# Kernel optimization log

Hardware: AMD Instinct MI355X
Metric: run time of the kernel (lower is better)

Reference implementation:

```python
import jax, jax.numpy as jnp
import numpy as np

D_IN = 1024
D_OUT = 1024

def setup_inputs() -> dict:
    key = jax.random.key(0)
    kx, kq, kk, kv = jax.random.split(key, 4)
    scale = 1.0 / np.sqrt(D_IN)
    return {
        "x": jax.random.normal(kx, (4, 4096, D_IN), dtype=jnp.float32),
        "W_q": jax.random.uniform(kq, (D_IN, D_OUT), dtype=jnp.float32, minval=-scale, maxval=scale),
        "W_k": jax.random.uniform(kk, (D_IN, D_OUT), dtype=jnp.float32, minval=-scale, maxval=scale),
        "W_v": jax.random.uniform(kv, (D_IN, D_OUT), dtype=jnp.float32, minval=-scale, maxval=scale),
    }

def reference(x, W_q, W_k, W_v):
    # x: [b, s, d_in]; weights stored as [d_in, d_out] (transposed vs torch Linear)
    Q = jnp.einsum('bsd,de->bse', x, W_q)
    K = jnp.einsum('bsd,de->bse', x, W_k)
    V = jnp.einsum('bsd,de->bse', x, W_v)
    d_k = K.shape[-1]
    scores = jnp.einsum('bqe,bke->bqk', Q, K) / jnp.sqrt(jnp.asarray(d_k, x.dtype))
    weights = jax.nn.softmax(scores, axis=-1)
    return jnp.einsum('bqk,bke->bqe', weights, V)
```

## Files before the change

kernel.cpp:

```cpp
#include <hip/hip_runtime.h>

typedef unsigned short u16;
typedef float f32x4 __attribute__((ext_vector_type(4)));
typedef u16   u16x4 __attribute__((ext_vector_type(4)));
typedef u16   u16x8 __attribute__((ext_vector_type(8)));
typedef __bf16 bf16x8 __attribute__((ext_vector_type(8)));

static __device__ __forceinline__ u16 f2bf(float x) {
    unsigned int u = __builtin_bit_cast(unsigned int, x);
    u = (u + 0x7FFFu + ((u >> 16) & 1u)) >> 16;
    return (u16)u;
}
static __device__ __forceinline__ bf16x8 as_bf(u16x8 v) { return __builtin_bit_cast(bf16x8, v); }

static __device__ __forceinline__ void gload16(const u16* g, u16* lds) {
    __builtin_amdgcn_global_load_lds(
        (const __attribute__((address_space(1))) void*)g,
        (__attribute__((address_space(3))) void*)lds,
        16, 0, 0);
}

#define KSCALE 0.045084220027780106f

#define STAGE_G2L(dst, src, stride, ROUNDS) do {                               \
    _Pragma("unroll") for (int i_ = 0; i_ < (ROUNDS); ++i_) {                  \
        int c_ = (i_ * 4 + w) * 64 + l;                                        \
        int row_ = c_ >> 3, c8_ = c_ & 7;                                      \
        gload16((src) + (size_t)row_ * (stride) + ((c8_ ^ (row_ & 7)) << 3),   \
                &(dst)[(i_ * 4 + w) * 512]);                                   \
    } } while (0)

__global__ __launch_bounds__(256) void wt_kernel(const float* __restrict__ Wq,
                                                 const float* __restrict__ Wk,
                                                 const float* __restrict__ Wv,
                                                 u16* __restrict__ Wt) {
    __shared__ float tile[64][65];
    const int mat = blockIdx.z;
    const float* W = (mat == 0) ? Wq : ((mat == 1) ? Wk : Wv);
    const int bx = blockIdx.x, by = blockIdx.y;
    const int tid = threadIdx.x;
#pragma unroll
    for (int i = 0; i < 16; ++i) {
        int idx = i * 256 + tid;
        int r = idx >> 6, c = idx & 63;
        tile[r][c] = W[(by * 64 + r) * 1024 + bx * 64 + c];
    }
    __syncthreads();
#pragma unroll
    for (int i = 0; i < 16; ++i) {
        int idx = i * 256 + tid;
        int r = idx >> 6, c = idx & 63;
        Wt[mat * 1048576 + (bx * 64 + r) * 1024 + by * 64 + c] = f2bf(tile[c][r]);
    }
}

__global__ __launch_bounds__(256, 3) void qkv_gemm(const float* __restrict__ X,
                                                   const u16* __restrict__ Wt,
                                                   u16* __restrict__ Qo,
                                                   u16* __restrict__ Ko,
                                                   u16* __restrict__ Vt) {
    __shared__ u16 As[128 * 64];
    __shared__ u16 Bs[128 * 64];
    const int bid = blockIdx.x;
    const int swz = (bid & 7) * 96 + (bid >> 3);
    const int bm = swz / 24, bn = swz % 24;
    const int tid = threadIdx.x;
    const int w = tid >> 6, l = tid & 63, lg = l >> 4, lr = l & 15;
    const int wr = w >> 1, wc = w & 1;

    const f32x4 z4 = {0.f, 0.f, 0.f, 0.f};
    f32x4 acc[4][4];
#pragma unroll
    for (int m = 0; m < 4; ++m)
#pragma unroll
        for (int n = 0; n < 4; ++n) acc[m][n] = z4;

    for (int kb = 0; kb < 16; ++kb) {
        __syncthreads();
        STAGE_G2L(Bs, Wt + (size_t)(bn * 128) * 1024 + kb * 64, 1024, 4);
#pragma unroll
        for (int i = 0; i < 4; ++i) {
            int cid = i * 256 + tid;
            int row = cid >> 3, c8 = cid & 7;
            const float* src = X + (bm * 128 + row) * 1024 + kb * 64 + c8 * 8;
            f32x4 v0 = *(const f32x4*)(src);
            f32x4 v1 = *(const f32x4*)(src + 4);
            u16x8 t;
            t[0] = f2bf(v0[0]); t[1] = f2bf(v0[1]); t[2] = f2bf(v0[2]); t[3] = f2bf(v0[3]);
            t[4] = f2bf(v1[0]); t[5] = f2bf(v1[1]); t[6] = f2bf(v1[2]); t[7] = f2bf(v1[3]);
            *(u16x8*)(&As[row * 64 + ((c8 ^ (row & 7)) << 3)]) = t;
        }
        __syncthreads();
#pragma unroll
        for (int kk = 0; kk < 2; ++kk) {
            bf16x8 af[4], bfr[4];
#pragma unroll
            for (int m = 0; m < 4; ++m) {
                int row = wr * 64 + m * 16 + lr;
                af[m] = as_bf(*(const u16x8*)(&As[row * 64 + (((kk * 4 + lg) ^ (lr & 7)) << 3)]));
            }
#pragma unroll
            for (int n = 0; n < 4; ++n) {
                int row = wc * 64 + n * 16 + lr;
                bfr[n] = as_bf(*(const u16x8*)(&Bs[row * 64 + (((kk * 4 + lg) ^ (lr & 7)) << 3)]));
            }
#pragma unroll
            for (int m = 0; m < 4; ++m)
#pragma unroll
                for (int n = 0; n < 4; ++n)
                    acc[m][n] = __builtin_amdgcn_mfma_f32_16x16x32_bf16(af[m], bfr[n], acc[m][n], 0, 0, 0);
        }
    }
    const int row0 = bm * 128 + wr * 64;
    const int col0 = bn * 128 + wc * 64;
#pragma unroll
    for (int m = 0; m < 4; ++m) {
#pragma unroll
        for (int n = 0; n < 4; ++n) {
            int col = col0 + n * 16 + lr;
            int mat = col >> 10;
            int cg = col & 1023;
            int row = row0 + m * 16 + lg * 4;
            if (mat == 2) {
                u16x4 v;
                v[0] = f2bf(acc[m][n][0]); v[1] = f2bf(acc[m][n][1]);
                v[2] = f2bf(acc[m][n][2]); v[3] = f2bf(acc[m][n][3]);
                *(u16x4*)(Vt + cg * 4096 + row) = v;
            } else {
                u16* P = mat ? Ko : Qo;
#pragma unroll
                for (int r = 0; r < 4; ++r) P[(row + r) * 1024 + cg] = f2bf(acc[m][n][r]);
            }
        }
    }
}

__global__ __launch_bounds__(256, 4) void qk_gemm(const u16* __restrict__ Qb,
                                                  const u16* __restrict__ Kb,
                                                  u16* __restrict__ P) {
    __shared__ u16 As[128 * 64];
    __shared__ u16 Bs[128 * 64];
    const int bid = blockIdx.x;
    const int swz = (bid & 7) * 128 + (bid >> 3);
    const int bm = swz >> 5, bn = swz & 31;
    const int tid = threadIdx.x;
    const int w = tid >> 6, l = tid & 63, lg = l >> 4, lr = l & 15;
    const int wr = w >> 1, wc = w & 1;

    const f32x4 z4 = {0.f, 0.f, 0.f, 0.f};
    f32x4 acc[4][4];
#pragma unroll
    for (int m = 0; m < 4; ++m)
#pragma unroll
        for (int n = 0; n < 4; ++n) acc[m][n] = z4;

    for (int kb = 0; kb < 16; ++kb) {
        __syncthreads();
        STAGE_G2L(As, Qb + (size_t)(bm * 128) * 1024 + kb * 64, 1024, 4);
        STAGE_G2L(Bs, Kb + (size_t)(bn * 128) * 1024 + kb * 64, 1024, 4);
        __syncthreads();
#pragma unroll
        for (int kk = 0; kk < 2; ++kk) {
            bf16x8 af[4], bfr[4];
#pragma unroll
            for (int m = 0; m < 4; ++m) {
                int row = wr * 64 + m * 16 + lr;
                af[m] = as_bf(*(const u16x8*)(&As[row * 64 + (((kk * 4 + lg) ^ (lr & 7)) << 3)]));
            }
#pragma unroll
            for (int n = 0; n < 4; ++n) {
                int row = wc * 64 + n * 16 + lr;
                bfr[n] = as_bf(*(const u16x8*)(&Bs[row * 64 + (((kk * 4 + lg) ^ (lr & 7)) << 3)]));
            }
#pragma unroll
            for (int m = 0; m < 4; ++m)
#pragma unroll
                for (int n = 0; n < 4; ++n)
                    acc[m][n] = __builtin_amdgcn_mfma_f32_16x16x32_bf16(af[m], bfr[n], acc[m][n], 0, 0, 0);
        }
    }
    const int row0 = bm * 128 + wr * 64;
    const int col0 = bn * 128 + wc * 64;
#pragma unroll
    for (int m = 0; m < 4; ++m) {
#pragma unroll
        for (int r = 0; r < 4; ++r) {
            const size_t rowg = (size_t)(row0 + m * 16 + lg * 4 + r);
#pragma unroll
            for (int n = 0; n < 4; ++n)
                P[rowg * 4096 + col0 + n * 16 + lr] = f2bf(exp2f(acc[m][n][r] * KSCALE));
        }
    }
}

__global__ __launch_bounds__(256, 4) void pv_pair(const u16* __restrict__ P0,
                                                  const u16* __restrict__ P1,
                                                  const u16* __restrict__ V0,
                                                  const u16* __restrict__ V1,
                                                  float* __restrict__ Out0,
                                                  float* __restrict__ Out1) {
    __shared__ u16 As[128 * 64];
    __shared__ u16 Bs[128 * 64];
    const int bid = blockIdx.x;
    const int swz = (bid & 7) * 64 + (bid >> 3);
    const int bb = swz >> 8, rem = swz & 255;
    const int bm = rem >> 3, bn = rem & 7;
    const int q0 = bm * 128, e0 = bn * 128;
    const u16* P  = bb ? P1 : P0;
    const u16* Vt = bb ? V1 : V0;
    float* Out    = bb ? Out1 : Out0;
    const int tid = threadIdx.x;
    const int w = tid >> 6, l = tid & 63, lg = l >> 4, lr = l & 15;
    const int wr = w >> 1, wc = w & 1;

    u16x8 ones_u;
#pragma unroll
    for (int i = 0; i < 8; ++i) ones_u[i] = 0x3F80;
    const bf16x8 ones8 = as_bf(ones_u);

    const f32x4 z4 = {0.f, 0.f, 0.f, 0.f};
    f32x4 acc[4][4];
    f32x4 acc_sum[4];
#pragma unroll
    for (int m = 0; m < 4; ++m) {
        acc_sum[m] = z4;
#pragma unroll
        for (int n = 0; n < 4; ++n) acc[m][n] = z4;
    }

    for (int kb = 0; kb < 64; ++kb) {
        __syncthreads();
        STAGE_G2L(As, P + (size_t)q0 * 4096 + kb * 64, 4096, 4);
        STAGE_G2L(Bs, Vt + (size_t)e0 * 4096 + kb * 64, 4096, 4);
        __syncthreads();
#pragma unroll
        for (int kk = 0; kk < 2; ++kk) {
            bf16x8 af[4], bfr[4];
#pragma unroll
            for (int m = 0; m < 4; ++m) {
                int row = wr * 64 + m * 16 + lr;
                af[m] = as_bf(*(const u16x8*)(&As[row * 64 + (((kk * 4 + lg) ^ (lr & 7)) << 3)]));
            }
#pragma unroll
            for (int n = 0; n < 4; ++n) {
                int row = wc * 64 + n * 16 + lr;
                bfr[n] = as_bf(*(const u16x8*)(&Bs[row * 64 + (((kk * 4 + lg) ^ (lr & 7)) << 3)]));
            }
#pragma unroll
            for (int m = 0; m < 4; ++m) {
#pragma unroll
                for (int n = 0; n < 4; ++n)
                    acc[m][n] = __builtin_amdgcn_mfma_f32_16x16x32_bf16(af[m], bfr[n], acc[m][n], 0, 0, 0);
                acc_sum[m] = __builtin_amdgcn_mfma_f32_16x16x32_bf16(af[m], ones8, acc_sum[m], 0, 0, 0);
            }
        }
    }
#pragma unroll
    for (int m = 0; m < 4; ++m) {
#pragma unroll
        for (int r = 0; r < 4; ++r) {
            int rloc = wr * 64 + m * 16 + lg * 4 + r;
            float rl = 1.0f / acc_sum[m][r];
#pragma unroll
            for (int n = 0; n < 4; ++n)
                Out[(size_t)(q0 + rloc) * 1024 + e0 + wc * 64 + n * 16 + lr] = acc[m][n][r] * rl;
        }
    }
}

extern "C" void kernel_launch(void* const* d_in, const int* in_sizes, int n_in,
                              void* d_out, int out_size, void* d_ws, size_t ws_size,
                              hipStream_t stream) {
    const float* x  = (const float*)d_in[0];
    const float* Wq = (const float*)d_in[1];
    const float* Wk = (const float*)d_in[2];
    const float* Wv = (const float*)d_in[3];
    float* out = (float*)d_out;

    char* ws = (char*)d_ws;
    u16* Wt = (u16*)(ws);
    u16* Qb = (u16*)(ws + 6291456);
    u16* Kb = (u16*)(ws + 14680064);
    u16* V0 = (u16*)(ws + 23068672);
    u16* V1 = (u16*)(ws + 31457280);
    u16* P0 = (u16*)(ws + 39845888);
    u16* P1 = (u16*)(ws + 73400320);

    wt_kernel<<<dim3(16, 16, 3), 256, 0, stream>>>(Wq, Wk, Wv, Wt);
    for (int p = 0; p < 2; ++p) {
        const float* x0 = x + (size_t)(2 * p) * 4194304;
        const float* x1 = x + (size_t)(2 * p + 1) * 4194304;
        float* o0 = out + (size_t)(2 * p) * 4194304;
        float* o1 = out + (size_t)(2 * p + 1) * 4194304;
        qkv_gemm<<<dim3(768), 256, 0, stream>>>(x0, Wt, Qb, Kb, V0);
        qk_gemm<<<dim3(1024), 256, 0, stream>>>(Qb, Kb, P0);
        qkv_gemm<<<dim3(768), 256, 0, stream>>>(x1, Wt, Qb, Kb, V1);
        qk_gemm<<<dim3(1024), 256, 0, stream>>>(Qb, Kb, P1);
        pv_pair<<<dim3(512), 256, 0, stream>>>(P0, P1, V0, V1, o0, o1);
    }
}
```

Baseline: 476.0 us.

## Compute softmax row sums in QK epilogue and double K-step in PV

The QK kernel now sums the bf16-rounded exponentials of each row slice with wave shuffles and writes partial sums to a workspace buffer. The PV kernel reads and reduces these partials instead of running an extra MFMA against a ones vector each step. PV also stages two 64-wide K chunks per barrier pair, halving the number of synchronizations. The cost is doubled LDS use, with launch bounds lowered to 2 blocks per CU, so occupancy drops.

```diff
diff --git a/kernel.cpp b/kernel.cpp
--- a/kernel.cpp
+++ b/kernel.cpp
@@ -10,6 +10,10 @@
     unsigned int u = __builtin_bit_cast(unsigned int, x);
     u = (u + 0x7FFFu + ((u >> 16) & 1u)) >> 16;
     return (u16)u;
+}
+static __device__ __forceinline__ float bf2f(u16 x) {
+    unsigned int u = ((unsigned int)x) << 16;
+    return __builtin_bit_cast(float, u);
 }
 static __device__ __forceinline__ bf16x8 as_bf(u16x8 v) { return __builtin_bit_cast(bf16x8, v); }
 
@@ -137,7 +141,8 @@
 
 __global__ __launch_bounds__(256, 4) void qk_gemm(const u16* __restrict__ Qb,
                                                   const u16* __restrict__ Kb,
-                                                  u16* __restrict__ P) {
+                                                  u16* __restrict__ P,
+                                                  float* __restrict__ pl) {
     __shared__ u16 As[128 * 64];
     __shared__ u16 Bs[128 * 64];
     const int bid = blockIdx.x;
@@ -186,21 +191,34 @@
 #pragma unroll
         for (int r = 0; r < 4; ++r) {
             const size_t rowg = (size_t)(row0 + m * 16 + lg * 4 + r);
-#pragma unroll
-            for (int n = 0; n < 4; ++n)
-                P[rowg * 4096 + col0 + n * 16 + lr] = f2bf(exp2f(acc[m][n][r] * KSCALE));
-        }
-    }
-}
-
-__global__ __launch_bounds__(256, 4) void pv_pair(const u16* __restrict__ P0,
+            float se = 0.f;
+#pragma unroll
+            for (int n = 0; n < 4; ++n) {
+                u16 pb = f2bf(exp2f(acc[m][n][r] * KSCALE));
+                P[rowg * 4096 + col0 + n * 16 + lr] = pb;
+                se += bf2f(pb);
+            }
+            se += __shfl_xor(se, 1, 64);
+            se += __shfl_xor(se, 2, 64);
+            se += __shfl_xor(se, 4, 64);
+            se += __shfl_xor(se, 8, 64);
+            if (lr == 0) pl[rowg * 64 + bn * 2 + wc] = se;
+        }
+    }
+}
+
+__global__ __launch_bounds__(256, 2) void pv_pair(const u16* __restrict__ P0,
                                                   const u16* __restrict__ P1,
                                                   const u16* __restrict__ V0,
                                                   const u16* __restrict__ V1,
+                                                  const float* __restrict__ pl,
                                                   float* __restrict__ Out0,
                                                   float* __restrict__ Out1) {
-    __shared__ u16 As[128 * 64];
-    __shared__ u16 Bs[128 * 64];
+    __shared__ u16 As0[128 * 64];
+    __shared__ u16 As1[128 * 64];
+    __shared__ u16 Bs0[128 * 64];
+    __shared__ u16 Bs1[128 * 64];
+    __shared__ float rl_s[128];
     const int bid = blockIdx.x;
     const int swz = (bid & 7) * 64 + (bid >> 3);
     const int bb = swz >> 8, rem = swz & 255;
@@ -213,46 +231,49 @@
     const int w = tid >> 6, l = tid & 63, lg = l >> 4, lr = l & 15;
     const int wr = w >> 1, wc = w & 1;
 
-    u16x8 ones_u;
-#pragma unroll
-    for (int i = 0; i < 8; ++i) ones_u[i] = 0x3F80;
-    const bf16x8 ones8 = as_bf(ones_u);
+    if (tid < 128) {
+        const f32x4* pp = (const f32x4*)(pl + (size_t)(bb * 4096 + q0 + tid) * 64);
+        f32x4 a = pp[0];
+#pragma unroll
+        for (int i = 1; i < 16; ++i) a += pp[i];
+        rl_s[tid] = 1.0f / (a[0] + a[1] + a[2] + a[3]);
+    }
 
     const f32x4 z4 = {0.f, 0.f, 0.f, 0.f};
     f32x4 acc[4][4];
-    f32x4 acc_sum[4];
-#pragma unroll
-    for (int m = 0; m < 4; ++m) {
-        acc_sum[m] = z4;
+#pragma unroll
+    for (int m = 0; m < 4; ++m)
 #pragma unroll
         for (int n = 0; n < 4; ++n) acc[m][n] = z4;
-    }
-
-    for (int kb = 0; kb < 64; ++kb) {
-        __syncthreads();
-        STAGE_G2L(As, P + (size_t)q0 * 4096 + kb * 64, 4096, 4);
-        STAGE_G2L(Bs, Vt + (size_t)e0 * 4096 + kb * 64, 4096, 4);
-        __syncthreads();
-#pragma unroll
-        for (int kk = 0; kk < 2; ++kk) {
+
+    for (int kb = 0; kb < 32; ++kb) {
+        __syncthreads();
+        STAGE_G2L(As0, P  + (size_t)q0 * 4096 + kb * 128,      4096, 4);
+        STAGE_G2L(As1, P  + (size_t)q0 * 4096 + kb * 128 + 64, 4096, 4);
+        STAGE_G2L(Bs0, Vt + (size_t)e0 * 4096 + kb * 128,      4096, 4);
+        STAGE_G2L(Bs1, Vt + (size_t)e0 * 4096 + kb * 128 + 64, 4096, 4);
+        __syncthreads();
+#pragma unroll
+        for (int g = 0; g < 4; ++g) {
+            const u16* Aa = (g < 2) ? As0 : As1;
+            const u16* Ba = (g < 2) ? Bs0 : Bs1;
+            const int kk = g & 1;
             bf16x8 af[4], bfr[4];
 #pragma unroll
             for (int m = 0; m < 4; ++m) {
                 int row = wr * 64 + m * 16 + lr;
-                af[m] = as_bf(*(const u16x8*)(&As[row * 64 + (((kk * 4 + lg) ^ (lr & 7)) << 3)]));
+                af[m] = as_bf(*(const u16x8*)(&Aa[row * 64 + (((kk * 4 + lg) ^ (lr & 7)) << 3)]));
             }
 #pragma unroll
             for (int n = 0; n < 4; ++n) {
                 int row = wc * 64 + n * 16 + lr;
-                bfr[n] = as_bf(*(const u16x8*)(&Bs[row * 64 + (((kk * 4 + lg) ^ (lr & 7)) << 3)]));
-            }
-#pragma unroll
-            for (int m = 0; m < 4; ++m) {
+                bfr[n] = as_bf(*(const u16x8*)(&Ba[row * 64 + (((kk * 4 + lg) ^ (lr & 7)) << 3)]));
+            }
+#pragma unroll
+            for (int m = 0; m < 4; ++m)
 #pragma unroll
                 for (int n = 0; n < 4; ++n)
                     acc[m][n] = __builtin_amdgcn_mfma_f32_16x16x32_bf16(af[m], bfr[n], acc[m][n], 0, 0, 0);
-                acc_sum[m] = __builtin_amdgcn_mfma_f32_16x16x32_bf16(af[m], ones8, acc_sum[m], 0, 0, 0);
-            }
         }
     }
 #pragma unroll
@@ -260,7 +281,7 @@
 #pragma unroll
         for (int r = 0; r < 4; ++r) {
             int rloc = wr * 64 + m * 16 + lg * 4 + r;
-            float rl = 1.0f / acc_sum[m][r];
+            float rl = rl_s[rloc];
 #pragma unroll
             for (int n = 0; n < 4; ++n)
                 Out[(size_t)(q0 + rloc) * 1024 + e0 + wc * 64 + n * 16 + lr] = acc[m][n][r] * rl;
@@ -278,13 +299,14 @@
     float* out = (float*)d_out;
 
     char* ws = (char*)d_ws;
-    u16* Wt = (u16*)(ws);
-    u16* Qb = (u16*)(ws + 6291456);
-    u16* Kb = (u16*)(ws + 14680064);
-    u16* V0 = (u16*)(ws + 23068672);
-    u16* V1 = (u16*)(ws + 31457280);
-    u16* P0 = (u16*)(ws + 39845888);
-    u16* P1 = (u16*)(ws + 73400320);
+    u16*   Wt  = (u16*)(ws);
+    u16*   Qb  = (u16*)(ws + 6291456);
+    u16*   Kb  = (u16*)(ws + 14680064);
+    u16*   V0  = (u16*)(ws + 23068672);
+    u16*   V1  = (u16*)(ws + 31457280);
+    u16*   P0  = (u16*)(ws + 39845888);
+    u16*   P1  = (u16*)(ws + 73400320);
+    float* plg = (float*)(ws + 106954752);
 
     wt_kernel<<<dim3(16, 16, 3), 256, 0, stream>>>(Wq, Wk, Wv, Wt);
     for (int p = 0; p < 2; ++p) {
@@ -293,9 +315,9 @@
         float* o0 = out + (size_t)(2 * p) * 4194304;
         float* o1 = out + (size_t)(2 * p + 1) * 4194304;
         qkv_gemm<<<dim3(768), 256, 0, stream>>>(x0, Wt, Qb, Kb, V0);
-        qk_gemm<<<dim3(1024), 256, 0, stream>>>(Qb, Kb, P0);
+        qk_gemm<<<dim3(1024), 256, 0, stream>>>(Qb, Kb, P0, plg);
         qkv_gemm<<<dim3(768), 256, 0, stream>>>(x1, Wt, Qb, Kb, V1);
-        qk_gemm<<<dim3(1024), 256, 0, stream>>>(Qb, Kb, P1);
-        pv_pair<<<dim3(512), 256, 0, stream>>>(P0, P1, V0, V1, o0, o1);
-    }
-}
+        qk_gemm<<<dim3(1024), 256, 0, stream>>>(Qb, Kb, P1, plg + 262144);
+        pv_pair<<<dim3(512), 256, 0, stream>>>(P0, P1, V0, V1, plg, o0, o1);
+    }
+}
```

After: 462.0 us. 1.03x faster.
